# Performance work log

Hardware: AMD Instinct MI355X
Metric: run time of the kernel (lower is better)

Reference implementation:

```python
import jax, jax.numpy as jnp
import numpy as np

N = 8192
D_IN = 128
D_HID = 256  # hard-coded nn.Linear(input_dim, 256) in the module
D_OUT = 64
BN_EPS = 1e-5
LEAKY_SLOPE = 0.01


def setup_inputs() -> dict:
    key = jax.random.key(0)
    k_h, k_a, k_wt, k_wo = jax.random.split(key, 4)
    H = jax.random.normal(k_h, (N, D_IN), dtype=jnp.float32)
    # Fixed adjacency passed to __init__; values in [0,1) so mask=ceil(A*1e-5) is {0,1}
    A = jax.random.uniform(k_a, (N, N), dtype=jnp.float32)
    bn_weight = jnp.ones((D_IN,), jnp.float32)
    bn_bias = jnp.zeros((D_IN,), jnp.float32)
    W_theta = jax.random.normal(k_wt, (D_IN, D_HID), jnp.float32) * np.float32(1.0 / np.sqrt(D_IN))
    b_theta = jnp.zeros((D_HID,), jnp.float32)
    W_out = jax.random.normal(k_wo, (D_IN, D_OUT), jnp.float32) * np.float32(1.0 / np.sqrt(D_IN))
    b_out = jnp.zeros((D_OUT,), jnp.float32)
    return {"H": H, "A": A, "bn_weight": bn_weight, "bn_bias": bn_bias,
            "W_theta": W_theta, "b_theta": b_theta, "W_out": W_out, "b_out": b_out}


def reference(H, A, bn_weight, bn_bias, W_theta, b_theta, W_out, b_out):
    # BatchNorm1d in training mode: biased batch statistics over the node dim
    mean = jnp.mean(H, axis=0)
    var = jnp.mean(jnp.square(H - mean), axis=0)
    Hn = (H - mean) * jax.lax.rsqrt(var + BN_EPS) * bn_weight + bn_bias  # [N, D_IN]

    Hx = Hn @ W_theta + b_theta  # [N, 256]
    mask = jnp.ceil(A * 1e-5)    # constant {0,1} mask from fixed adjacency

    # Dynamic adjacency: clamp(sigmoid(Hx Hx^T), min=0.1) * mask + I
    S = jnp.clip(jax.nn.sigmoid(Hx @ Hx.T), 0.1, None)  # [N, N]
    Ad = S * mask + jnp.eye(N, dtype=H.dtype)

    # D^{-1/2} A D^{-1/2} via broadcast scaling (same math as diag matmuls)
    d = jax.lax.rsqrt(jnp.sum(Ad, axis=1))  # D^{-0.5}, [N]
    A_hat = Ad * d[:, None] * d[None, :]

    out = A_hat @ (Hn @ W_out + b_out)       # [N, D_OUT]
    out = jnp.where(out >= 0, out, LEAKY_SLOPE * out)  # LeakyReLU(0.01)
    return out, A_hat
```

## Files before the change

### kernel.cpp

```cpp
#include <hip/hip_runtime.h>
#include <hip/hip_bf16.h>

#define N 8192
#define DIN 128
#define DHID 256
#define DOUT 64
#define LDP 72
#define VP 136

typedef __attribute__((ext_vector_type(8))) short short8;
typedef __attribute__((ext_vector_type(8))) unsigned short u16x8;
typedef __attribute__((ext_vector_type(4))) float f32x4;
typedef __attribute__((ext_vector_type(2))) float f32x2;

typedef __attribute__((address_space(1))) const unsigned int GlbU32;
typedef __attribute__((address_space(3))) unsigned int LdsU32;

__device__ inline void gload16(const void* g, void* l) {
  __builtin_amdgcn_global_load_lds((GlbU32*)g, (LdsU32*)l, 16, 0, 0);
}

#define LGKM_BAR()                                            \
  do {                                                        \
    asm volatile("s_waitcnt lgkmcnt(0)" ::: "memory");        \
    __builtin_amdgcn_sched_barrier(0);                        \
    __builtin_amdgcn_s_barrier();                             \
    __builtin_amdgcn_sched_barrier(0);                        \
  } while (0)

__device__ inline unsigned short f2bf(float x) {
  unsigned u = __float_as_uint(x);
  u += 0x7FFF + ((u >> 16) & 1);
  return (unsigned short)(u >> 16);
}
__device__ inline float bf2f(unsigned short u) {
  return __uint_as_float(((unsigned)u) << 16);
}
__device__ inline float sig_clip(float x) {
  float s = 1.0f / (1.0f + __expf(-x));
  return fmaxf(s, 0.1f);
}

__global__ void bn_stats(const float* __restrict__ H, const float* __restrict__ bnw,
                         const float* __restrict__ bnb, float* __restrict__ scale,
                         float* __restrict__ shift) {
  int f = blockIdx.x;
  int t = threadIdx.x;
  float s = 0.f, sq = 0.f;
  for (int r = t; r < N; r += 256) {
    float v = H[(size_t)r * DIN + f];
    s += v; sq += v * v;
  }
  __shared__ float ss[256], s2[256];
  ss[t] = s; s2[t] = sq;
  __syncthreads();
  for (int o = 128; o > 0; o >>= 1) {
    if (t < o) { ss[t] += ss[t + o]; s2[t] += s2[t + o]; }
    __syncthreads();
  }
  if (t == 0) {
    float mean = ss[0] * (1.0f / N);
    float var = s2[0] * (1.0f / N) - mean * mean;
    float sc = rsqrtf(var + 1e-5f) * bnw[f];
    scale[f] = sc;
    shift[f] = bnb[f] - mean * sc;
  }
}

__global__ __launch_bounds__(256) void proj(const float* __restrict__ H,
                     const float* __restrict__ scale, const float* __restrict__ shift,
                     const float* __restrict__ Wt, const float* __restrict__ bt,
                     const float* __restrict__ Wo, const float* __restrict__ bo,
                     unsigned short* __restrict__ Hx, unsigned short* __restrict__ M2T) {
  __shared__ float hn[8][DIN];
  int i0 = blockIdx.x * 8;
  int t = threadIdx.x;
  #pragma unroll
  for (int rep = 0; rep < 4; ++rep) {
    int idx = rep * 256 + t;
    int r = idx >> 7, c = idx & 127;
    float h = H[(size_t)(i0 + r) * DIN + c];
    hn[r][c] = fmaf(h, scale[c], shift[c]);
  }
  __syncthreads();
  {
    int c = t;
    float acc[8];
    float b = bt[c];
    #pragma unroll
    for (int r = 0; r < 8; ++r) acc[r] = b;
    for (int k = 0; k < DIN; ++k) {
      float w = Wt[k * DHID + c];
      #pragma unroll
      for (int r = 0; r < 8; ++r) acc[r] = fmaf(hn[r][k], w, acc[r]);
    }
    #pragma unroll
    for (int r = 0; r < 8; ++r) Hx[(size_t)(i0 + r) * DHID + c] = f2bf(acc[r]);
  }
  if (t < DOUT) {
    int c = t;
    float acc[8];
    float b = bo[c];
    #pragma unroll
    for (int r = 0; r < 8; ++r) acc[r] = b;
    for (int k = 0; k < DIN; ++k) {
      float w = Wo[k * DOUT + c];
      #pragma unroll
      for (int r = 0; r < 8; ++r) acc[r] = fmaf(hn[r][k], w, acc[r]);
    }
    u16x8 v;
    #pragma unroll
    for (int r = 0; r < 8; ++r) v[r] = f2bf(acc[r]);
    *(u16x8*)&M2T[(size_t)c * N + i0] = v;
  }
}

__global__ __launch_bounds__(256) void smat(const unsigned short* __restrict__ Hx,
                     const float* __restrict__ A,
                     float* __restrict__ rowsum,
                     unsigned short* __restrict__ Vout) {
  int jt = blockIdx.x, it = blockIdx.y;
  if (jt < it) return;
  __shared__ unsigned short lsh[17408];
  __shared__ unsigned mbt32[128][4];
  __shared__ unsigned mbtT[128][4];
  unsigned short* la = lsh;
  unsigned short* lb = lsh + 8192;
  float* scs = (float*)mbt32;
  int i0 = it * 128, j0 = jt * 128;
  int t = threadIdx.x;
  int w = t >> 6, l = t & 63;
  int lr = l & 15, lg = l >> 4;
  const bool offdiag = (it != jt);

  f32x4 acc[2][8];
  f32x4 zero = {0.f, 0.f, 0.f, 0.f};
  #pragma unroll
  for (int m = 0; m < 2; ++m)
    #pragma unroll
    for (int n = 0; n < 8; ++n) acc[m][n] = zero;

  const int srow = l >> 3;
  const int scol = ((l & 7) ^ srow) * 8;
  const int fswz = (lr & 7) * 8;

  for (int c4 = 0; c4 < 4; ++c4) {
    int k0 = c4 * 64;
    __syncthreads();
    #pragma unroll
    for (int rp = 0; rp < 4; ++rp) {
      int chunk = rp * 4 + w;
      int row = chunk * 8 + srow;
      gload16(&Hx[(size_t)(i0 + row) * DHID + k0 + scol], &la[chunk * 512]);
      gload16(&Hx[(size_t)(j0 + row) * DHID + k0 + scol], &lb[chunk * 512]);
    }
    const int rbase = w * 32 + c4 * 8;
    f32x2 au[8], al[8];
    #pragma unroll
    for (int rr = 0; rr < 8; ++rr)
      au[rr] = *(const f32x2*)&A[(size_t)(i0 + rbase + rr) * N + j0 + 2 * l];
    if (offdiag) {
      #pragma unroll
      for (int rr = 0; rr < 8; ++rr)
        al[rr] = *(const f32x2*)&A[(size_t)(j0 + rbase + rr) * N + i0 + 2 * l];
    }
    __syncthreads();
    #pragma unroll
    for (int rr = 0; rr < 8; ++rr) {
      unsigned long long be = __ballot(au[rr][0] > 0.f);
      unsigned long long bo = __ballot(au[rr][1] > 0.f);
      if (l == 0) {
        mbt32[rbase + rr][0] = (unsigned)be;
        mbt32[rbase + rr][1] = (unsigned)(be >> 32);
        mbt32[rbase + rr][2] = (unsigned)bo;
        mbt32[rbase + rr][3] = (unsigned)(bo >> 32);
      }
    }
    if (offdiag) {
      #pragma unroll
      for (int rr = 0; rr < 8; ++rr) {
        unsigned long long be = __ballot(al[rr][0] > 0.f);
        unsigned long long bo = __ballot(al[rr][1] > 0.f);
        if (l == 0) {
          mbtT[rbase + rr][0] = (unsigned)be;
          mbtT[rbase + rr][1] = (unsigned)(be >> 32);
          mbtT[rbase + rr][2] = (unsigned)bo;
          mbtT[rbase + rr][3] = (unsigned)(bo >> 32);
        }
      }
    }
    #pragma unroll
    for (int kk = 0; kk < 2; ++kk) {
      int c = (kk * 32 + lg * 8) ^ fswz;
      short8 af[2], bf[8];
      #pragma unroll
      for (int m = 0; m < 2; ++m)
        af[m] = *(const short8*)&la[(w * 32 + m * 16 + lr) * 64 + c];
      #pragma unroll
      for (int n = 0; n < 8; ++n)
        bf[n] = *(const short8*)&lb[(n * 16 + lr) * 64 + c];
      #pragma unroll
      for (int m = 0; m < 2; ++m)
        #pragma unroll
        for (int n = 0; n < 8; ++n)
          acc[m][n] = __builtin_amdgcn_mfma_f32_16x16x32_bf16(af[m], bf[n], acc[m][n], 0, 0, 0);
    }
  }

  LGKM_BAR();

  #pragma unroll
  for (int m = 0; m < 2; ++m) {
    #pragma unroll
    for (int r = 0; r < 4; ++r) {
      int rl = w * 32 + m * 16 + lg * 4 + r;
      int gi = i0 + rl;
      unsigned w0 = mbt32[rl][(lr & 1) * 2];
      unsigned w1 = mbt32[rl][(lr & 1) * 2 + 1];
      float part = 0.f;
      #pragma unroll
      for (int n = 0; n < 8; ++n) {
        int gj = j0 + n * 16 + lr;
        float s = sig_clip(acc[m][n][r]);
        acc[m][n][r] = s;
        unsigned mwv = (n < 4) ? w0 : w1;
        float ms = ((mwv >> ((n & 3) * 8 + (lr >> 1))) & 1u) ? 1.f : 0.f;
        float v = s * ms + (gi == gj ? 1.f : 0.f);
        part += v;
        lsh[rl * VP + n * 16 + lr] = f2bf(v);
      }
      part += __shfl_xor(part, 1);
      part += __shfl_xor(part, 2);
      part += __shfl_xor(part, 4);
      part += __shfl_xor(part, 8);
      if (lr == 0) atomicAdd(&rowsum[gi], part);
    }
  }

  LGKM_BAR();
  #pragma unroll
  for (int pass = 0; pass < 8; ++pass) {
    int row = pass * 16 + (t >> 4);
    int cc = (t & 15) * 8;
    u16x8 vv = *(const u16x8*)&lsh[row * VP + cc];
    *(u16x8*)&Vout[(size_t)(i0 + row) * N + j0 + cc] = vv;
  }

  if (offdiag) {
    LGKM_BAR();
    float p[8];
    #pragma unroll
    for (int n = 0; n < 8; ++n) p[n] = 0.f;
    #pragma unroll
    for (int m = 0; m < 2; ++m) {
      #pragma unroll
      for (int r = 0; r < 4; ++r) {
        int rl = w * 32 + m * 16 + lg * 4 + r;
        int wi = (r & 1) * 2 + (w >> 1);
        int bitp = (w & 1) * 16 + m * 8 + lg * 2 + (r >> 1);
        #pragma unroll
        for (int n = 0; n < 8; ++n) {
          int c = n * 16 + lr;
          float ms = ((mbtT[c][wi] >> bitp) & 1u) ? 1.f : 0.f;
          float v = acc[m][n][r] * ms;
          p[n] += v;
          lsh[c * VP + rl] = f2bf(v);
        }
      }
    }
    #pragma unroll
    for (int n = 0; n < 8; ++n) {
      p[n] += __shfl_xor(p[n], 16);
      p[n] += __shfl_xor(p[n], 32);
    }
    if (lg == 0) {
      #pragma unroll
      for (int n = 0; n < 8; ++n) scs[w * 128 + n * 16 + lr] = p[n];
    }
    LGKM_BAR();
    if (t < 128) {
      float cs = scs[0 * 128 + t] + scs[1 * 128 + t] + scs[2 * 128 + t] + scs[3 * 128 + t];
      atomicAdd(&rowsum[j0 + t], cs);
    }
    #pragma unroll
    for (int pass = 0; pass < 8; ++pass) {
      int row = pass * 16 + (t >> 4);
      int cc = (t & 15) * 8;
      u16x8 vv = *(const u16x8*)&lsh[row * VP + cc];
      *(u16x8*)&Vout[(size_t)(j0 + row) * N + i0 + cc] = vv;
    }
  }
}

__global__ void dfin(float* rs) {
  int i = blockIdx.x * 256 + threadIdx.x;
  if (i < N) rs[i] = rsqrtf(rs[i]);
}

__global__ __launch_bounds__(256) void outmm(const unsigned short* __restrict__ Vin,
                      const float* __restrict__ dd,
                      const unsigned short* __restrict__ M2T,
                      float* __restrict__ Ahat, float* __restrict__ out) {
  __shared__ unsigned short la[2][128 * LDP];
  int kc = blockIdx.x;
  int it = blockIdx.y;
  int i0 = it * 128;
  int jbase = kc * 512;
  int t = threadIdx.x;
  int w = t >> 6, l = t & 63;
  int lr = l & 15, lg = l >> 4;

  f32x4 acc[2][4];
  f32x4 zero = {0.f, 0.f, 0.f, 0.f};
  #pragma unroll
  for (int m = 0; m < 2; ++m)
    #pragma unroll
    for (int n = 0; n < 4; ++n) acc[m][n] = zero;

  const unsigned short* V = (const unsigned short*)Vin;
  const int row8 = t >> 3;
  const int cc8 = (t & 7) * 8;

  float di[4];
  #pragma unroll
  for (int rep = 0; rep < 4; ++rep) di[rep] = dd[i0 + rep * 32 + row8];

  u16x8 u[2][4];
  #pragma unroll
  for (int rep = 0; rep < 4; ++rep)
    u[0][rep] = *(const u16x8*)&V[(size_t)(i0 + rep * 32 + row8) * N + jbase + cc8];

  #pragma unroll
  for (int s = 0; s < 8; ++s) {
    const int cur = s & 1;
    const int j0 = jbase + s * 64;
    if (s < 7) {
      #pragma unroll
      for (int rep = 0; rep < 4; ++rep)
        u[cur ^ 1][rep] = *(const u16x8*)&V[(size_t)(i0 + rep * 32 + row8) * N + j0 + 64 + cc8];
    }
    short8 bfr[2][4];
    #pragma unroll
    for (int kk = 0; kk < 2; ++kk)
      #pragma unroll
      for (int n = 0; n < 4; ++n)
        bfr[kk][n] = *(const short8*)&M2T[(size_t)(n * 16 + lr) * N + j0 + kk * 32 + lg * 8];
    f32x4 dj0 = *(const f32x4*)&dd[j0 + cc8];
    f32x4 dj1 = *(const f32x4*)&dd[j0 + cc8 + 4];
    #pragma unroll
    for (int rep = 0; rep < 4; ++rep) {
      int row = rep * 32 + row8;
      size_t idx = (size_t)(i0 + row) * N + j0 + cc8;
      f32x4 s0, s1;
      s0[0] = bf2f(u[cur][rep][0]) * di[rep] * dj0[0];
      s0[1] = bf2f(u[cur][rep][1]) * di[rep] * dj0[1];
      s0[2] = bf2f(u[cur][rep][2]) * di[rep] * dj0[2];
      s0[3] = bf2f(u[cur][rep][3]) * di[rep] * dj0[3];
      s1[0] = bf2f(u[cur][rep][4]) * di[rep] * dj1[0];
      s1[1] = bf2f(u[cur][rep][5]) * di[rep] * dj1[1];
      s1[2] = bf2f(u[cur][rep][6]) * di[rep] * dj1[2];
      s1[3] = bf2f(u[cur][rep][7]) * di[rep] * dj1[3];
      *(f32x4*)&Ahat[idx] = s0;
      *(f32x4*)&Ahat[idx + 4] = s1;
      u16x8 b;
      b[0] = f2bf(s0[0]); b[1] = f2bf(s0[1]); b[2] = f2bf(s0[2]); b[3] = f2bf(s0[3]);
      b[4] = f2bf(s1[0]); b[5] = f2bf(s1[1]); b[6] = f2bf(s1[2]); b[7] = f2bf(s1[3]);
      *(u16x8*)&la[cur][row * LDP + cc8] = b;
    }
    LGKM_BAR();
    #pragma unroll
    for (int kk = 0; kk < 2; ++kk) {
      short8 af[2];
      #pragma unroll
      for (int m = 0; m < 2; ++m)
        af[m] = *(const short8*)&la[cur][(w * 32 + m * 16 + lr) * LDP + kk * 32 + lg * 8];
      #pragma unroll
      for (int m = 0; m < 2; ++m)
        #pragma unroll
        for (int n = 0; n < 4; ++n)
          acc[m][n] = __builtin_amdgcn_mfma_f32_16x16x32_bf16(af[m], bfr[kk][n], acc[m][n], 0, 0, 0);
    }
  }

  #pragma unroll
  for (int m = 0; m < 2; ++m)
    #pragma unroll
    for (int n = 0; n < 4; ++n)
      #pragma unroll
      for (int r = 0; r < 4; ++r) {
        int gi = i0 + w * 32 + m * 16 + lg * 4 + r;
        int gc = n * 16 + lr;
        atomicAdd(&out[(size_t)gi * DOUT + gc], acc[m][n][r]);
      }
}

__global__ void leaky(float* out) {
  int i = blockIdx.x * 256 + threadIdx.x;
  if (i < N * DOUT) {
    float x = out[i];
    out[i] = x >= 0.f ? x : 0.01f * x;
  }
}

extern "C" void kernel_launch(void* const* d_in, const int* in_sizes, int n_in,
                              void* d_out, int out_size, void* d_ws, size_t ws_size,
                              hipStream_t stream) {
  const float* H   = (const float*)d_in[0];
  const float* A   = (const float*)d_in[1];
  const float* bnw = (const float*)d_in[2];
  const float* bnb = (const float*)d_in[3];
  const float* Wt  = (const float*)d_in[4];
  const float* bt  = (const float*)d_in[5];
  const float* Wo  = (const float*)d_in[6];
  const float* bo  = (const float*)d_in[7];
  float* out = (float*)d_out;
  float* Ahat = out + (size_t)N * DOUT;

  char* ws = (char*)d_ws;
  float* scale  = (float*)(ws + 0);
  float* shift  = (float*)(ws + 512);
  float* rowsum = (float*)(ws + 4096);
  unsigned short* M2T = (unsigned short*)(ws + 65536);
  unsigned short* Hx  = (unsigned short*)(ws + 2097152);
  unsigned short* Vbf = (unsigned short*)(ws + (size_t)(14u << 20));

  hipMemsetAsync(rowsum, 0, N * sizeof(float), stream);
  hipMemsetAsync(out, 0, (size_t)N * DOUT * sizeof(float), stream);

  bn_stats<<<DIN, 256, 0, stream>>>(H, bnw, bnb, scale, shift);
  proj<<<N / 8, 256, 0, stream>>>(H, scale, shift, Wt, bt, Wo, bo, Hx, M2T);
  smat<<<dim3(64, 64), 256, 0, stream>>>(Hx, A, rowsum, Vbf);
  dfin<<<N / 256, 256, 0, stream>>>(rowsum);
  outmm<<<dim3(16, 64), 256, 0, stream>>>(Vbf, rowsum, M2T, Ahat, out);
  leaky<<<(N * DOUT + 255) / 256, 256, 0, stream>>>(out);
}
```

Baseline: 308.6 us.

## Stage Hx K-dimension in two halves and hoist mask loads out of MFMA loop

The smat kernel now loads half of the Hx K-range (two 64-wide chunks) into larger LDS buffers at once, so it needs only two load/sync phases instead of four. The A-mask loads and ballots for both the tile and its transpose move before the first MFMA phase, where they overlap with the Hx global-to-LDS copies. The padded VP-stride staging for the output tile becomes an XOR-swizzled 128-stride layout inside lb. Doubling LDS per block (about 64KB) may lower occupancy, and the A loads are no longer spread across the K loop.

```diff
diff --git a/kernel.cpp b/kernel.cpp
--- a/kernel.cpp
+++ b/kernel.cpp
@@ -6,7 +6,6 @@
 #define DHID 256
 #define DOUT 64
 #define LDP 72
-#define VP 136
 
 typedef __attribute__((ext_vector_type(8))) short short8;
 typedef __attribute__((ext_vector_type(8))) unsigned short u16x8;
@@ -121,11 +120,10 @@
                      unsigned short* __restrict__ Vout) {
   int jt = blockIdx.x, it = blockIdx.y;
   if (jt < it) return;
-  __shared__ unsigned short lsh[17408];
+  __shared__ unsigned short la[16384];
+  __shared__ unsigned short lb[16384];
   __shared__ unsigned mbt32[128][4];
   __shared__ unsigned mbtT[128][4];
-  unsigned short* la = lsh;
-  unsigned short* lb = lsh + 8192;
   float* scs = (float*)mbt32;
   int i0 = it * 128, j0 = jt * 128;
   int t = threadIdx.x;
@@ -133,38 +131,32 @@
   int lr = l & 15, lg = l >> 4;
   const bool offdiag = (it != jt);
 
-  f32x4 acc[2][8];
-  f32x4 zero = {0.f, 0.f, 0.f, 0.f};
-  #pragma unroll
-  for (int m = 0; m < 2; ++m)
-    #pragma unroll
-    for (int n = 0; n < 8; ++n) acc[m][n] = zero;
-
   const int srow = l >> 3;
   const int scol = ((l & 7) ^ srow) * 8;
   const int fswz = (lr & 7) * 8;
 
-  for (int c4 = 0; c4 < 4; ++c4) {
-    int k0 = c4 * 64;
-    __syncthreads();
-    #pragma unroll
-    for (int rp = 0; rp < 4; ++rp) {
-      int chunk = rp * 4 + w;
-      int row = chunk * 8 + srow;
-      gload16(&Hx[(size_t)(i0 + row) * DHID + k0 + scol], &la[chunk * 512]);
-      gload16(&Hx[(size_t)(j0 + row) * DHID + k0 + scol], &lb[chunk * 512]);
-    }
-    const int rbase = w * 32 + c4 * 8;
-    f32x2 au[8], al[8];
+  f32x4 acc[2][8];
+  f32x4 zero = {0.f, 0.f, 0.f, 0.f};
+  #pragma unroll
+  for (int m = 0; m < 2; ++m)
+    #pragma unroll
+    for (int n = 0; n < 8; ++n) acc[m][n] = zero;
+
+  #pragma unroll
+  for (int idx4 = 0; idx4 < 8; ++idx4) {
+    int idx = idx4 * 4 + w;
+    int c4l = idx >> 4, rg = idx & 15;
+    int row = rg * 8 + srow;
+    gload16(&Hx[(size_t)(i0 + row) * DHID + c4l * 64 + scol], &la[c4l * 8192 + rg * 512]);
+    gload16(&Hx[(size_t)(j0 + row) * DHID + c4l * 64 + scol], &lb[c4l * 8192 + rg * 512]);
+  }
+  #pragma unroll
+  for (int g = 0; g < 4; ++g) {
+    const int rbase = w * 32 + g * 8;
+    f32x2 au[8];
     #pragma unroll
     for (int rr = 0; rr < 8; ++rr)
       au[rr] = *(const f32x2*)&A[(size_t)(i0 + rbase + rr) * N + j0 + 2 * l];
-    if (offdiag) {
-      #pragma unroll
-      for (int rr = 0; rr < 8; ++rr)
-        al[rr] = *(const f32x2*)&A[(size_t)(j0 + rbase + rr) * N + i0 + 2 * l];
-    }
-    __syncthreads();
     #pragma unroll
     for (int rr = 0; rr < 8; ++rr) {
       unsigned long long be = __ballot(au[rr][0] > 0.f);
@@ -176,7 +168,15 @@
         mbt32[rbase + rr][3] = (unsigned)(bo >> 32);
       }
     }
-    if (offdiag) {
+  }
+  if (offdiag) {
+    #pragma unroll
+    for (int g = 0; g < 4; ++g) {
+      const int rbase = w * 32 + g * 8;
+      f32x2 al[8];
+      #pragma unroll
+      for (int rr = 0; rr < 8; ++rr)
+        al[rr] = *(const f32x2*)&A[(size_t)(j0 + rbase + rr) * N + i0 + 2 * l];
       #pragma unroll
       for (int rr = 0; rr < 8; ++rr) {
         unsigned long long be = __ballot(al[rr][0] > 0.f);
@@ -189,16 +189,52 @@
         }
       }
     }
+  }
+  __syncthreads();
+
+  #pragma unroll
+  for (int c4l = 0; c4l < 2; ++c4l) {
     #pragma unroll
     for (int kk = 0; kk < 2; ++kk) {
       int c = (kk * 32 + lg * 8) ^ fswz;
       short8 af[2], bf[8];
       #pragma unroll
       for (int m = 0; m < 2; ++m)
-        af[m] = *(const short8*)&la[(w * 32 + m * 16 + lr) * 64 + c];
+        af[m] = *(const short8*)&la[c4l * 8192 + (w * 32 + m * 16 + lr) * 64 + c];
       #pragma unroll
       for (int n = 0; n < 8; ++n)
-        bf[n] = *(const short8*)&lb[(n * 16 + lr) * 64 + c];
+        bf[n] = *(const short8*)&lb[c4l * 8192 + (n * 16 + lr) * 64 + c];
+      #pragma unroll
+      for (int m = 0; m < 2; ++m)
+        #pragma unroll
+        for (int n = 0; n < 8; ++n)
+          acc[m][n] = __builtin_amdgcn_mfma_f32_16x16x32_bf16(af[m], bf[n], acc[m][n], 0, 0, 0);
+    }
+  }
+  LGKM_BAR();
+
+  #pragma unroll
+  for (int idx4 = 0; idx4 < 8; ++idx4) {
+    int idx = idx4 * 4 + w;
+    int c4l = idx >> 4, rg = idx & 15;
+    int row = rg * 8 + srow;
+    gload16(&Hx[(size_t)(i0 + row) * DHID + (2 + c4l) * 64 + scol], &la[c4l * 8192 + rg * 512]);
+    gload16(&Hx[(size_t)(j0 + row) * DHID + (2 + c4l) * 64 + scol], &lb[c4l * 8192 + rg * 512]);
+  }
+  __syncthreads();
+
+  #pragma unroll
+  for (int c4l = 0; c4l < 2; ++c4l) {
+    #pragma unroll
+    for (int kk = 0; kk < 2; ++kk) {
+      int c = (kk * 32 + lg * 8) ^ fswz;
+      short8 af[2], bf[8];
+      #pragma unroll
+      for (int m = 0; m < 2; ++m)
+        af[m] = *(const short8*)&la[c4l * 8192 + (w * 32 + m * 16 + lr) * 64 + c];
+      #pragma unroll
+      for (int n = 0; n < 8; ++n)
+        bf[n] = *(const short8*)&lb[c4l * 8192 + (n * 16 + lr) * 64 + c];
       #pragma unroll
       for (int m = 0; m < 2; ++m)
         #pragma unroll
@@ -218,6 +254,7 @@
       unsigned w0 = mbt32[rl][(lr & 1) * 2];
       unsigned w1 = mbt32[rl][(lr & 1) * 2 + 1];
       float part = 0.f;
+      int rsw = (rl & 7) << 3;
       #pragma unroll
       for (int n = 0; n < 8; ++n) {
         int gj = j0 + n * 16 + lr;
@@ -227,7 +264,7 @@
         float ms = ((mwv >> ((n & 3) * 8 + (lr >> 1))) & 1u) ? 1.f : 0.f;
         float v = s * ms + (gi == gj ? 1.f : 0.f);
         part += v;
-        lsh[rl * VP + n * 16 + lr] = f2bf(v);
+        lb[rl * 128 + ((n * 16 + lr) ^ rsw)] = f2bf(v);
       }
       part += __shfl_xor(part, 1);
       part += __shfl_xor(part, 2);
@@ -242,7 +279,7 @@
   for (int pass = 0; pass < 8; ++pass) {
     int row = pass * 16 + (t >> 4);
     int cc = (t & 15) * 8;
-    u16x8 vv = *(const u16x8*)&lsh[row * VP + cc];
+    u16x8 vv = *(const u16x8*)&lb[row * 128 + (cc ^ ((row & 7) << 3))];
     *(u16x8*)&Vout[(size_t)(i0 + row) * N + j0 + cc] = vv;
   }
 
@@ -264,7 +301,7 @@
           float ms = ((mbtT[c][wi] >> bitp) & 1u) ? 1.f : 0.f;
           float v = acc[m][n][r] * ms;
           p[n] += v;
-          lsh[c * VP + rl] = f2bf(v);
+          lb[c * 128 + (rl ^ ((c & 7) << 3))] = f2bf(v);
         }
       }
     }
@@ -286,7 +323,7 @@
     for (int pass = 0; pass < 8; ++pass) {
       int row = pass * 16 + (t >> 4);
       int cc = (t & 15) * 8;
-      u16x8 vv = *(const u16x8*)&lsh[row * VP + cc];
+      u16x8 vv = *(const u16x8*)&lb[row * 128 + (cc ^ ((row & 7) << 3))];
       *(u16x8*)&Vout[(size_t)(j0 + row) * N + i0 + cc] = vv;
     }
   }
```

After: 319.3 us. +3.5%, slower.
